# Kernel tuning notes

Measured on AMD Instinct MI355X. Metric: run time of the kernel, lower is better.

Reference implementation:

```python
import jax, jax.numpy as jnp
import numpy as np

B, V = 256, 128000

def setup_inputs() -> dict:
    key = jax.random.key(0)
    k1, k2, k3 = jax.random.split(key, 3)
    logits = jax.random.normal(k1, (B, V), dtype=jnp.float32)
    # temperatures in [0,1); force a few exact zeros to exercise the greedy path
    temperatures = jax.random.uniform(k2, (B,), dtype=jnp.float32)
    temperatures = temperatures.at[:8].set(0.0)
    # uniform noise for Gumbel-max sampling (stand-in for torch.multinomial RNG)
    uniform_noise = jax.random.uniform(k3, (B, V), dtype=jnp.float32,
                                       minval=1e-7, maxval=1.0 - 1e-7)
    return {"logits": logits, "temperatures": temperatures, "uniform_noise": uniform_noise}

def reference(logits, temperatures, uniform_noise):
    logits = logits.astype(jnp.float32)
    greedy_tokens = jnp.argmax(logits, axis=-1)                     # [B]
    safe_t = jnp.where(temperatures == 0, jnp.ones_like(temperatures), temperatures)
    scaled = logits / safe_t[:, None]                               # [B, V]
    probs = jax.nn.softmax(scaled, axis=-1)                         # [B, V]
    # Gumbel-max trick: argmax(scaled + g), g ~ Gumbel(0,1) == multinomial(probs)
    gumbel = -jnp.log(-jnp.log(uniform_noise))
    sample_tokens = jnp.argmax(scaled + gumbel, axis=-1)            # [B]
    tokens = jnp.where(temperatures == 0, greedy_tokens, sample_tokens)
    return tokens, probs
```

## Files before the change

### kernel.cpp

```cpp
#include <hip/hip_runtime.h>
#include <math.h>

#define BATCH 256
#define VOCAB 128000
#define V4 (VOCAB / 4)
#define NTHREADS 1024
#define NWAVES (NTHREADS / 64)

typedef float vfloat4 __attribute__((ext_vector_type(4)));

__global__ __launch_bounds__(NTHREADS) void sampler_kernel(
    const float* __restrict__ logits,
    const float* __restrict__ temps,
    const float* __restrict__ noise,
    float* __restrict__ out_tokens,
    float* __restrict__ out_probs)
{
    const int b   = blockIdx.x;
    const int tid = threadIdx.x;
    const int wave = tid >> 6;
    const int lane = tid & 63;

    const float t      = temps[b];
    const float safe_t = (t == 0.0f) ? 1.0f : t;
    const float inv_t  = 1.0f / safe_t;

    const vfloat4* lg4 = (const vfloat4*)(logits + (size_t)b * VOCAB);
    const vfloat4* nz4 = (const vfloat4*)(noise  + (size_t)b * VOCAB);
    vfloat4*       pb4 = (vfloat4*)(out_probs + (size_t)b * VOCAB);

    float m = -INFINITY, s = 0.0f;
    float gv = -INFINITY; int gi = 0;

    for (int i = tid; i < V4; i += NTHREADS) {
        vfloat4 x4 = lg4[i];
#pragma unroll
        for (int j = 0; j < 4; ++j) {
            const int   idx = 4 * i + j;
            const float x   = x4[j];
            const float sc  = x * inv_t;
            if (x > gv) { gv = x; gi = idx; }
            const float mn = fmaxf(m, sc);
            s = s * __expf(m - mn) + __expf(sc - mn);
            m = mn;
        }
    }

#pragma unroll
    for (int off = 32; off >= 1; off >>= 1) {
        float m2  = __shfl_down(m,  off);
        float s2  = __shfl_down(s,  off);
        float gv2 = __shfl_down(gv, off);
        int   gi2 = __shfl_down(gi, off);
        float mn = fmaxf(m, m2);
        s = s * __expf(m - mn) + s2 * __expf(m2 - mn);
        m = mn;
        if (gv2 > gv || (gv2 == gv && gi2 < gi)) { gv = gv2; gi = gi2; }
    }

    __shared__ float sm[NWAVES], ss[NWAVES], sgv[NWAVES];
    __shared__ int   sgi[NWAVES];
    __shared__ float bM, binvS;
    __shared__ int   bGI;
    if (lane == 0) { sm[wave] = m; ss[wave] = s; sgv[wave] = gv; sgi[wave] = gi; }
    __syncthreads();
    if (tid == 0) {
        float M = sm[0], S = ss[0], GV = sgv[0]; int GI = sgi[0];
        for (int w = 1; w < NWAVES; ++w) {
            float mn = fmaxf(M, sm[w]);
            S = S * __expf(M - mn) + ss[w] * __expf(sm[w] - mn);
            M = mn;
            if (sgv[w] > GV || (sgv[w] == GV && sgi[w] < GI)) { GV = sgv[w]; GI = sgi[w]; }
        }
        bM = M; binvS = 1.0f / S; bGI = GI;
    }
    __syncthreads();
    const float M    = bM;
    const float invS = binvS;

    float sv = -INFINITY; int si = 0;

    for (int i = tid; i < V4; i += NTHREADS) {
        vfloat4 x4 = lg4[i];
        vfloat4 u4 = __builtin_nontemporal_load(&nz4[i]);
        vfloat4 p;
#pragma unroll
        for (int j = 0; j < 4; ++j) {
            const int   idx = 4 * i + j;
            const float sc  = x4[j] * inv_t;
            p[j] = __expf(sc - M) * invS;
            const float g = -__logf(-__logf(u4[j]));
            const float z = sc + g;
            if (z > sv) { sv = z; si = idx; }
        }
        __builtin_nontemporal_store(p, &pb4[i]);
    }

#pragma unroll
    for (int off = 32; off >= 1; off >>= 1) {
        float sv2 = __shfl_down(sv, off);
        int   si2 = __shfl_down(si, off);
        if (sv2 > sv || (sv2 == sv && si2 < si)) { sv = sv2; si = si2; }
    }
    __shared__ float ssv[NWAVES];
    __shared__ int   ssi[NWAVES];
    if (lane == 0) { ssv[wave] = sv; ssi[wave] = si; }
    __syncthreads();
    if (tid == 0) {
        float SV = ssv[0]; int SI = ssi[0];
        for (int w = 1; w < NWAVES; ++w) {
            if (ssv[w] > SV || (ssv[w] == SV && ssi[w] < SI)) { SV = ssv[w]; SI = ssi[w]; }
        }
        const int token = (t == 0.0f) ? bGI : SI;
        out_tokens[b] = (float)token;
    }
}

extern "C" void kernel_launch(void* const* d_in, const int* in_sizes, int n_in,
                              void* d_out, int out_size, void* d_ws, size_t ws_size,
                              hipStream_t stream) {
    const float* logits = (const float*)d_in[0];
    const float* temps  = (const float*)d_in[1];
    const float* noise  = (const float*)d_in[2];
    float* out = (float*)d_out;
    sampler_kernel<<<BATCH, NTHREADS, 0, stream>>>(logits, temps, noise,
                                                   out, out + BATCH);
}
```

Before: 321.2 us.

## Fuse Gumbel sampling into first pass and track raw-logit max for softmax

Moves the Gumbel-max sampling and noise read into the first pass, so the second pass only recomputes and writes probabilities and the separate sample reduction is dropped. The online softmax now keys on the raw-logit max, which is shared with the greedy argmax. It combines four elements before each rescale, so the per-element exp/max chain becomes one rescale per vector. Both loops are also unrolled by two with independent accumulators to increase memory-level parallelism. The cost is more registers, and the exp((gv-mn)*inv_t) form relies on a positive inv_t to keep the max correct.

```diff
diff --git a/kernel.cpp b/kernel.cpp
--- a/kernel.cpp
+++ b/kernel.cpp
@@ -16,8 +16,8 @@
     float* __restrict__ out_tokens,
     float* __restrict__ out_probs)
 {
-    const int b   = blockIdx.x;
-    const int tid = threadIdx.x;
+    const int b    = blockIdx.x;
+    const int tid  = threadIdx.x;
     const int wave = tid >> 6;
     const int lane = tid & 63;
 
@@ -29,90 +29,132 @@
     const vfloat4* nz4 = (const vfloat4*)(noise  + (size_t)b * VOCAB);
     vfloat4*       pb4 = (vfloat4*)(out_probs + (size_t)b * VOCAB);
 
-    float m = -INFINITY, s = 0.0f;
-    float gv = -INFINITY; int gi = 0;
+    float gv0 = -INFINITY, gv1 = -INFINITY;
+    int   gi0 = 0,          gi1 = 0;
+    float s0  = 0.0f,       s1  = 0.0f;
+    float sv0 = -INFINITY,  sv1 = -INFINITY;
+    int   si0 = 0,          si1 = 0;
 
-    for (int i = tid; i < V4; i += NTHREADS) {
-        vfloat4 x4 = lg4[i];
-#pragma unroll
-        for (int j = 0; j < 4; ++j) {
-            const int   idx = 4 * i + j;
-            const float x   = x4[j];
-            const float sc  = x * inv_t;
-            if (x > gv) { gv = x; gi = idx; }
-            const float mn = fmaxf(m, sc);
-            s = s * __expf(m - mn) + __expf(sc - mn);
-            m = mn;
-        }
+    auto proc1 = [&](const vfloat4 x4, const vfloat4 u4, int idx0,
+                     float& gv, int& gi, float& s, float& sv, int& si) {
+        float v01 = fmaxf(x4[0], x4[1]);
+        int   i01 = (x4[1] > x4[0]) ? idx0 + 1 : idx0;
+        float v23 = fmaxf(x4[2], x4[3]);
+        int   i23 = (x4[3] > x4[2]) ? idx0 + 3 : idx0 + 2;
+        float cm  = fmaxf(v01, v23);
+        int   cmi = (v23 > v01) ? i23 : i01;
+
+        float e0 = __expf((x4[0] - cm) * inv_t);
+        float e1 = __expf((x4[1] - cm) * inv_t);
+        float e2 = __expf((x4[2] - cm) * inv_t);
+        float e3 = __expf((x4[3] - cm) * inv_t);
+        float cs = (e0 + e1) + (e2 + e3);
+
+        float mn = fmaxf(gv, cm);
+        s = s * __expf((gv - mn) * inv_t) + cs * __expf((cm - mn) * inv_t);
+        if (cm > gv) gi = cmi;
+        gv = mn;
+
+        float g0 = -__logf(-__logf(u4[0]));
+        float g1 = -__logf(-__logf(u4[1]));
+        float g2 = -__logf(-__logf(u4[2]));
+        float g3 = -__logf(-__logf(u4[3]));
+        float z0 = x4[0] * inv_t + g0;
+        float z1 = x4[1] * inv_t + g1;
+        float z2 = x4[2] * inv_t + g2;
+        float z3 = x4[3] * inv_t + g3;
+        float w01 = fmaxf(z0, z1);
+        int   j01 = (z1 > z0) ? idx0 + 1 : idx0;
+        float w23 = fmaxf(z2, z3);
+        int   j23 = (z3 > z2) ? idx0 + 3 : idx0 + 2;
+        float wm  = fmaxf(w01, w23);
+        int   wmi = (w23 > w01) ? j23 : j01;
+        if (wm > sv) { si = wmi; sv = wm; }
+    };
+
+    int i = tid;
+    for (; i + NTHREADS < V4; i += 2 * NTHREADS) {
+        vfloat4 xa = lg4[i];
+        vfloat4 xb = lg4[i + NTHREADS];
+        vfloat4 ua = __builtin_nontemporal_load(&nz4[i]);
+        vfloat4 ub = __builtin_nontemporal_load(&nz4[i + NTHREADS]);
+        proc1(xa, ua, 4 * i,              gv0, gi0, s0, sv0, si0);
+        proc1(xb, ub, 4 * (i + NTHREADS), gv1, gi1, s1, sv1, si1);
+    }
+    if (i < V4) {
+        vfloat4 xa = lg4[i];
+        vfloat4 ua = __builtin_nontemporal_load(&nz4[i]);
+        proc1(xa, ua, 4 * i, gv0, gi0, s0, sv0, si0);
+    }
+
+    {
+        float mn = fmaxf(gv0, gv1);
+        s0 = s0 * __expf((gv0 - mn) * inv_t) + s1 * __expf((gv1 - mn) * inv_t);
+        if (gv1 > gv0 || (gv1 == gv0 && gi1 < gi0)) gi0 = gi1;
+        gv0 = mn;
+        if (sv1 > sv0 || (sv1 == sv0 && si1 < si0)) { sv0 = sv1; si0 = si1; }
     }
 
 #pragma unroll
     for (int off = 32; off >= 1; off >>= 1) {
-        float m2  = __shfl_down(m,  off);
-        float s2  = __shfl_down(s,  off);
-        float gv2 = __shfl_down(gv, off);
-        int   gi2 = __shfl_down(gi, off);
-        float mn = fmaxf(m, m2);
-        s = s * __expf(m - mn) + s2 * __expf(m2 - mn);
-        m = mn;
-        if (gv2 > gv || (gv2 == gv && gi2 < gi)) { gv = gv2; gi = gi2; }
+        float gv2 = __shfl_down(gv0, off);
+        int   gi2 = __shfl_down(gi0, off);
+        float s2  = __shfl_down(s0,  off);
+        float sv2 = __shfl_down(sv0, off);
+        int   si2 = __shfl_down(si0, off);
+        float mn = fmaxf(gv0, gv2);
+        s0 = s0 * __expf((gv0 - mn) * inv_t) + s2 * __expf((gv2 - mn) * inv_t);
+        if (gv2 > gv0 || (gv2 == gv0 && gi2 < gi0)) gi0 = gi2;
+        gv0 = mn;
+        if (sv2 > sv0 || (sv2 == sv0 && si2 < si0)) { sv0 = sv2; si0 = si2; }
     }
 
-    __shared__ float sm[NWAVES], ss[NWAVES], sgv[NWAVES];
-    __shared__ int   sgi[NWAVES];
-    __shared__ float bM, binvS;
-    __shared__ int   bGI;
-    if (lane == 0) { sm[wave] = m; ss[wave] = s; sgv[wave] = gv; sgi[wave] = gi; }
+    __shared__ float sh_gv[NWAVES], sh_s[NWAVES], sh_sv[NWAVES];
+    __shared__ int   sh_gi[NWAVES], sh_si[NWAVES];
+    __shared__ float bGV, binvS;
+    if (lane == 0) {
+        sh_gv[wave] = gv0; sh_s[wave] = s0; sh_gi[wave] = gi0;
+        sh_sv[wave] = sv0; sh_si[wave] = si0;
+    }
     __syncthreads();
     if (tid == 0) {
-        float M = sm[0], S = ss[0], GV = sgv[0]; int GI = sgi[0];
+        float GVr = sh_gv[0], S = sh_s[0], SV = sh_sv[0];
+        int   GI  = sh_gi[0], SI = sh_si[0];
         for (int w = 1; w < NWAVES; ++w) {
-            float mn = fmaxf(M, sm[w]);
-            S = S * __expf(M - mn) + ss[w] * __expf(sm[w] - mn);
-            M = mn;
-            if (sgv[w] > GV || (sgv[w] == GV && sgi[w] < GI)) { GV = sgv[w]; GI = sgi[w]; }
+            float mn = fmaxf(GVr, sh_gv[w]);
+            S = S * __expf((GVr - mn) * inv_t) + sh_s[w] * __expf((sh_gv[w] - mn) * inv_t);
+            if (sh_gv[w] > GVr || (sh_gv[w] == GVr && sh_gi[w] < GI)) GI = sh_gi[w];
+            GVr = mn;
+            if (sh_sv[w] > SV || (sh_sv[w] == SV && sh_si[w] < SI)) { SV = sh_sv[w]; SI = sh_si[w]; }
         }
-        bM = M; binvS = 1.0f / S; bGI = GI;
+        bGV = GVr; binvS = 1.0f / S;
+        out_tokens[b] = (float)((t == 0.0f) ? GI : SI);
     }
     __syncthreads();
-    const float M    = bM;
+    const float Msc  = bGV * inv_t;
     const float invS = binvS;
 
-    float sv = -INFINITY; int si = 0;
-
-    for (int i = tid; i < V4; i += NTHREADS) {
-        vfloat4 x4 = lg4[i];
-        vfloat4 u4 = __builtin_nontemporal_load(&nz4[i]);
-        vfloat4 p;
+    int k = tid;
+    for (; k + NTHREADS < V4; k += 2 * NTHREADS) {
+        vfloat4 xa = lg4[k];
+        vfloat4 xb = lg4[k + NTHREADS];
+        vfloat4 pa, pb;
 #pragma unroll
-        for (int j = 0; j < 4; ++j) {
-            const int   idx = 4 * i + j;
-            const float sc  = x4[j] * inv_t;
-            p[j] = __expf(sc - M) * invS;
-            const float g = -__logf(-__logf(u4[j]));
-            const float z = sc + g;
-            if (z > sv) { sv = z; si = idx; }
-        }
-        __builtin_nontemporal_store(p, &pb4[i]);
+        for (int j = 0; j < 4; ++j)
+            pa[j] = __expf(fmaf(xa[j], inv_t, -Msc)) * invS;
+#pragma unroll
+        for (int j = 0; j < 4; ++j)
+            pb[j] = __expf(fmaf(xb[j], inv_t, -Msc)) * invS;
+        __builtin_nontemporal_store(pa, &pb4[k]);
+        __builtin_nontemporal_store(pb, &pb4[k + NTHREADS]);
     }
-
+    if (k < V4) {
+        vfloat4 xa = lg4[k];
+        vfloat4 pa;
 #pragma unroll
-    for (int off = 32; off >= 1; off >>= 1) {
-        float sv2 = __shfl_down(sv, off);
-        int   si2 = __shfl_down(si, off);
-        if (sv2 > sv || (sv2 == sv && si2 < si)) { sv = sv2; si = si2; }
-    }
-    __shared__ float ssv[NWAVES];
-    __shared__ int   ssi[NWAVES];
-    if (lane == 0) { ssv[wave] = sv; ssi[wave] = si; }
-    __syncthreads();
-    if (tid == 0) {
-        float SV = ssv[0]; int SI = ssi[0];
-        for (int w = 1; w < NWAVES; ++w) {
-            if (ssv[w] > SV || (ssv[w] == SV && ssi[w] < SI)) { SV = ssv[w]; SI = ssi[w]; }
-        }
-        const int token = (t == 0.0f) ? bGI : SI;
-        out_tokens[b] = (float)token;
+        for (int j = 0; j < 4; ++j)
+            pa[j] = __expf(fmaf(xa[j], inv_t, -Msc)) * invS;
+        __builtin_nontemporal_store(pa, &pb4[k]);
     }
 }
 
```

New measurement: 321.9 us. Within noise of the previous version (+0.2%).
